# Optimization experiments

Measured on AMD Instinct MI355X. Metric: run time of the kernel, lower is better.

Reference implementation:

```python
import jax, jax.numpy as jnp
import numpy as np

N_EMBD = 1024
NUM_HEADS = 16
HEAD_SIZE = 64


def setup_inputs() -> dict:
    key = jax.random.key(0)
    ks = jax.random.split(key, 6)
    B, T, C, hs = 2, 2048, N_EMBD, HEAD_SIZE
    s = 0.02
    return {
        "x": jax.random.normal(ks[0], (B, T, C), dtype=jnp.float32),
        "Wk": jax.random.normal(ks[1], (hs, C), dtype=jnp.float32) * s,  # torch Linear weight [out,in]
        "Wv": jax.random.normal(ks[2], (hs, C), dtype=jnp.float32) * s,
        "Wq": jax.random.normal(ks[3], (C, C), dtype=jnp.float32) * s,
        "Wp": jax.random.normal(ks[4], (C, C), dtype=jnp.float32) * s,
        "bp": jax.random.normal(ks[5], (C,), dtype=jnp.float32) * s,
    }


def reference(x, Wk, Wv, Wq, Wp, bp):
    B, T, C = x.shape
    H, hs = NUM_HEADS, HEAD_SIZE
    k = x @ Wk.T                      # [B,T,hs]
    v = x @ Wv.T                      # [B,T,hs]
    q = x @ Wq.T                      # [B,T,C]
    # Faithful to torch: raw view of [B,T,C] -> [B,H,T,hs] (row-major reshape, not transpose)
    q = q.reshape(B, H, T, hs)
    k = k.reshape(B, 1, T, hs)
    v = v.reshape(B, 1, T, hs)
    att = jnp.einsum("bhqd,bhkd->bhqk", q, jnp.broadcast_to(k, (B, 1, T, hs))) * (hs ** -0.5)
    mask = jnp.tril(jnp.ones((T, T), dtype=bool))[None, None]  # [1,1,T,T]
    att = jnp.where(mask, att, -jnp.inf)
    att = jax.nn.softmax(att, axis=-1)
    y = jnp.einsum("bhqk,bhkd->bhqd", att, jnp.broadcast_to(v, (B, 1, T, hs)))  # [B,H,T,hs]
    y = jnp.transpose(y, (0, 2, 1, 3)).reshape(B, T, C)
    return y @ Wp.T + bp
```

## Files before the change

### kernel.cpp

```cpp
#include <hip/hip_runtime.h>
#include <cstddef>
#include <cstdint>

#define B_N 2
#define T_N 2048
#define C_N 1024
#define H_N 16
#define HS_N 64
#define M_N (B_N * T_N)

typedef __attribute__((ext_vector_type(8))) short bf16x8;
typedef __attribute__((ext_vector_type(4))) float f32x4;

#define QSCALE 0.18033688011112042f

__device__ __forceinline__ ushort f2bf(float f) {
    union { float f; uint32_t u; } v; v.f = f;
    uint32_t r = v.u + 0x7fffu + ((v.u >> 16) & 1u);
    return (ushort)(r >> 16);
}
__device__ __forceinline__ ushort f2bf_trunc(float f) {
    union { float f; uint32_t u; } v; v.f = f;
    return (ushort)(v.u >> 16);
}

#define GLL16(g, l)                                                         \
    __builtin_amdgcn_global_load_lds(                                       \
        (const __attribute__((address_space(1))) unsigned int*)(g),         \
        (__attribute__((address_space(3))) unsigned int*)(l), 16, 0, 0)

__global__ void cvt_all_kernel(const float* __restrict__ x,
                               const float* __restrict__ Wq,
                               const float* __restrict__ Wp,
                               const float* __restrict__ Wk,
                               const float* __restrict__ Wv,
                               ushort* __restrict__ xb,
                               ushort* __restrict__ Wqb,
                               ushort* __restrict__ Wpb,
                               ushort* __restrict__ Wkvb) {
    const int S0 = M_N * C_N / 4;
    const int S1 = S0 + C_N * C_N / 4;
    const int S2 = S1 + C_N * C_N / 4;
    const int S3 = S2 + HS_N * C_N / 4;
    const int S4 = S3 + HS_N * C_N / 4;
    const int stride = gridDim.x * blockDim.x;
    for (int i = blockIdx.x * blockDim.x + threadIdx.x; i < S4; i += stride) {
        const float* src; ushort* dst; int j; float sc = 1.f;
        if (i < S0)      { src = x;  dst = xb;   j = i; }
        else if (i < S1) { src = Wq; dst = Wqb;  j = i - S0; sc = QSCALE; }
        else if (i < S2) { src = Wp; dst = Wpb;  j = i - S1; }
        else if (i < S3) { src = Wk; dst = Wkvb; j = i - S2; }
        else             { src = Wv; dst = Wkvb + HS_N * C_N; j = i - S3; }
        const float4 f = ((const float4*)src)[j];
        ushort4 o;
        o.x = f2bf(f.x * sc); o.y = f2bf(f.y * sc);
        o.z = f2bf(f.z * sc); o.w = f2bf(f.w * sc);
        ((ushort4*)dst)[j] = o;
    }
}

template <int MODE>
__global__ __launch_bounds__(256, 2) void gemm_bf16(
    const ushort* __restrict__ A,
    const ushort* __restrict__ W,
    const float* __restrict__ bias,
    void* __restrict__ Cout,
    ushort* __restrict__ kb,
    ushort* __restrict__ vbt,
    int K)
{
    __shared__ ushort As[64 * 64];
    __shared__ ushort Bs[128 * 64];
    const int flat = blockIdx.x + (blockIdx.y << 6);
    const int m0 = (((flat & 7) << 3) | ((flat >> 3) & 7)) * 64;
    const int n0 = (flat >> 6) * 128;
    const int tid = threadIdx.x;
    const int wid = tid >> 6;
    const int lane = tid & 63;
    const int ln = lane & 15;
    const int quad = lane >> 4;
    const int wm = wid >> 1, wn = wid & 1;

    f32x4 acc[2][4];
    #pragma unroll
    for (int i = 0; i < 2; ++i)
        #pragma unroll
        for (int j = 0; j < 4; ++j)
            acc[i][j] = (f32x4){0.f, 0.f, 0.f, 0.f};

    const int srow = lane >> 3;
    const int schk = (lane & 7) ^ srow;

    for (int k0 = 0; k0 < K; k0 += 64) {
        __syncthreads();
        #pragma unroll
        for (int t = 0; t < 2; ++t) {
            const int seg = wid * 2 + t;
            GLL16(A + (size_t)(m0 + seg * 8 + srow) * K + k0 + schk * 8,
                  As + seg * 512);
        }
        #pragma unroll
        for (int t = 0; t < 4; ++t) {
            const int seg = wid * 4 + t;
            GLL16(W + (size_t)(n0 + seg * 8 + srow) * K + k0 + schk * 8,
                  Bs + seg * 512);
        }
        __syncthreads();

        #pragma unroll
        for (int hh = 0; hh < 2; ++hh) {
            bf16x8 af[2], bf[4];
            const int sw = ln & 7;
            #pragma unroll
            for (int i = 0; i < 2; ++i) {
                const int row = wm * 32 + i * 16 + ln;
                af[i] = *(const bf16x8*)&As[row * 64 + (((hh * 4 + quad) ^ sw) * 8)];
            }
            #pragma unroll
            for (int j = 0; j < 4; ++j) {
                const int row = wn * 64 + j * 16 + ln;
                bf[j] = *(const bf16x8*)&Bs[row * 64 + (((hh * 4 + quad) ^ sw) * 8)];
            }
            #pragma unroll
            for (int i = 0; i < 2; ++i)
                #pragma unroll
                for (int j = 0; j < 4; ++j)
                    acc[i][j] = __builtin_amdgcn_mfma_f32_16x16x32_bf16(
                        af[i], bf[j], acc[i][j], 0, 0, 0);
        }
    }

    if (MODE == 1 && n0 >= C_N) {
        #pragma unroll
        for (int i = 0; i < 2; ++i) {
            const int row0 = m0 + wm * 32 + i * 16 + quad * 4;
            #pragma unroll
            for (int j = 0; j < 4; ++j) {
                const int c2 = wn * 64 + j * 16 + ln;
                if (c2 >= 64) {
                    const int d = c2 - 64;
                    const int b = row0 >> 11;
                    const int t0 = row0 & 2047;
                    ushort4 pk;
                    pk.x = f2bf(acc[i][j][0]); pk.y = f2bf(acc[i][j][1]);
                    pk.z = f2bf(acc[i][j][2]); pk.w = f2bf(acc[i][j][3]);
                    *(ushort4*)&vbt[((size_t)b * 64 + d) * T_N + t0] = pk;
                } else {
                    #pragma unroll
                    for (int reg = 0; reg < 4; ++reg)
                        kb[(size_t)(row0 + reg) * 64 + c2] = f2bf(acc[i][j][reg]);
                }
            }
        }
        return;
    }

    #pragma unroll
    for (int i = 0; i < 2; ++i) {
        #pragma unroll
        for (int j = 0; j < 4; ++j) {
            const int col = n0 + wn * 64 + j * 16 + ln;
            const float bv = (MODE == 0) ? bias[col] : 0.f;
            #pragma unroll
            for (int reg = 0; reg < 4; ++reg) {
                const int row = m0 + wm * 32 + i * 16 + quad * 4 + reg;
                const float v = acc[i][j][reg] + bv;
                if (MODE == 0)
                    ((float*)Cout)[(size_t)row * C_N + col] = v;
                else
                    ((ushort*)Cout)[(size_t)row * C_N + col] = f2bf(v);
            }
        }
    }
}

__global__ __launch_bounds__(256, 2) void attn_mfma_kernel(
    const ushort* __restrict__ qb,
    const ushort* __restrict__ kb,
    const ushort* __restrict__ vbt,
    ushort* __restrict__ yb)
{
    __shared__ ushort Ks[64][72];
    __shared__ ushort Vt[64][72];
    __shared__ ushort Ps[4][16][72];

    const int bh = blockIdx.x;
    const int b = bh >> 4, h = bh & 15;
    const int p = blockIdx.y;
    const int qA0 = p * 64;
    const int qB0 = (31 - p) * 64;
    const int tid = threadIdx.x;
    const int wid = tid >> 6;
    const int lane = tid & 63;
    const int ln = lane & 15;
    const int quad = lane >> 4;

    const ushort* qstrip = qb + (size_t)b * T_N * C_N + (size_t)h * T_N * HS_N;
    const size_t rB = (size_t)(qB0 + wid * 16 + ln) * HS_N;
    const size_t rA = (size_t)(qA0 + wid * 16 + ln) * HS_N;
    bf16x8 qfB[2], qfA[2];
    qfB[0] = *(const bf16x8*)(qstrip + rB + quad * 8);
    qfB[1] = *(const bf16x8*)(qstrip + rB + 32 + quad * 8);
    qfA[0] = *(const bf16x8*)(qstrip + rA + quad * 8);
    qfA[1] = *(const bf16x8*)(qstrip + rA + 32 + quad * 8);

    f32x4 oB[4], oA[4];
    float lB = 0.f, lA = 0.f;
    #pragma unroll
    for (int nt = 0; nt < 4; ++nt) {
        oB[nt] = (f32x4){0.f, 0.f, 0.f, 0.f};
        oA[nt] = (f32x4){0.f, 0.f, 0.f, 0.f};
    }

    const ushort* kbase = kb + (size_t)b * T_N * HS_N;
    const ushort* vtbase = vbt + (size_t)b * HS_N * T_N;
    const int rs = tid >> 3;
    const int cs = tid & 7;

    int4 kc0, kc1, vc0, vc1;
    {
        kc0 = *(const int4*)(kbase + (size_t)rs * HS_N + cs * 8);
        kc1 = *(const int4*)(kbase + (size_t)(rs + 32) * HS_N + cs * 8);
        vc0 = *(const int4*)(vtbase + (size_t)rs * T_N + cs * 8);
        vc1 = *(const int4*)(vtbase + (size_t)(rs + 32) * T_N + cs * 8);
    }

    bf16x8 kf[4][2], vf[4][2];

    auto tile_compute = [&](const bf16x8* qf, f32x4* o, float& l,
                            int qt0, int k0) {
        const int qs0 = qt0 + wid * 16;
        const int qg = qs0 + ln;
        f32x4 sc[4];
        #pragma unroll
        for (int nt = 0; nt < 4; ++nt) {
            sc[nt] = (f32x4){0.f, 0.f, 0.f, 0.f};
            sc[nt] = __builtin_amdgcn_mfma_f32_16x16x32_bf16(
                kf[nt][0], qf[0], sc[nt], 0, 0, 0);
            sc[nt] = __builtin_amdgcn_mfma_f32_16x16x32_bf16(
                kf[nt][1], qf[1], sc[nt], 0, 0, 0);
        }
        const bool dg = (k0 + 63 > qs0);
        #pragma unroll
        for (int nt = 0; nt < 4; ++nt) {
            ushort pk[4];
            #pragma unroll
            for (int reg = 0; reg < 4; ++reg) {
                const int key = k0 + nt * 16 + quad * 4 + reg;
                float sv = sc[nt][reg];
                if (dg && key > qg) sv = -1e30f;
                const float pe = __builtin_amdgcn_exp2f(sv);
                l += pe;
                pk[reg] = f2bf_trunc(pe);
            }
            *(uint2*)&Ps[wid][ln][nt * 16 + quad * 4] = *(const uint2*)pk;
        }
        #pragma unroll
        for (int ks2 = 0; ks2 < 2; ++ks2) {
            const bf16x8 pf = *(const bf16x8*)&Ps[wid][ln][ks2 * 32 + quad * 8];
            #pragma unroll
            for (int nt = 0; nt < 4; ++nt)
                o[nt] = __builtin_amdgcn_mfma_f32_16x16x32_bf16(
                    pf, vf[nt][ks2], o[nt], 0, 0, 0);
        }
    };

    const int nkt = 32 - p;
    for (int kt = 0; kt < nkt; ++kt) {
        const int k0 = kt * 64;
        __syncthreads();
        *(int4*)&Ks[rs][cs * 8] = kc0;
        *(int4*)&Ks[rs + 32][cs * 8] = kc1;
        *(int4*)&Vt[rs][cs * 8] = vc0;
        *(int4*)&Vt[rs + 32][cs * 8] = vc1;
        __syncthreads();
        if (kt + 1 < nkt) {
            const int kn = k0 + 64;
            kc0 = *(const int4*)(kbase + (size_t)(kn + rs) * HS_N + cs * 8);
            kc1 = *(const int4*)(kbase + (size_t)(kn + rs + 32) * HS_N + cs * 8);
            vc0 = *(const int4*)(vtbase + (size_t)rs * T_N + kn + cs * 8);
            vc1 = *(const int4*)(vtbase + (size_t)(rs + 32) * T_N + kn + cs * 8);
        }
        #pragma unroll
        for (int nt = 0; nt < 4; ++nt) {
            kf[nt][0] = *(const bf16x8*)&Ks[nt * 16 + ln][quad * 8];
            kf[nt][1] = *(const bf16x8*)&Ks[nt * 16 + ln][32 + quad * 8];
            vf[nt][0] = *(const bf16x8*)&Vt[nt * 16 + ln][quad * 8];
            vf[nt][1] = *(const bf16x8*)&Vt[nt * 16 + ln][32 + quad * 8];
        }
        tile_compute(qfB, oB, lB, qB0, k0);
        if (kt <= p)
            tile_compute(qfA, oA, lA, qA0, k0);
    }

    #pragma unroll
    for (int t = 0; t < 2; ++t) {
        float l = t ? lA : lB;
        const f32x4* o = t ? oA : oB;
        const int qt0 = t ? qA0 : qB0;
        l += __shfl_xor(l, 16);
        l += __shfl_xor(l, 32);
        #pragma unroll
        for (int reg = 0; reg < 4; ++reg) {
            const float inv = 1.0f / __shfl(l, quad * 4 + reg);
            const int qg = qt0 + wid * 16 + quad * 4 + reg;
            ushort* yrow = yb + (size_t)b * T_N * C_N + (size_t)qg * C_N
                           + h * HS_N;
            #pragma unroll
            for (int nt = 0; nt < 4; ++nt)
                yrow[nt * 16 + ln] = f2bf(o[nt][reg] * inv);
        }
    }
}

extern "C" void kernel_launch(void* const* d_in, const int* in_sizes, int n_in,
                              void* d_out, int out_size, void* d_ws, size_t ws_size,
                              hipStream_t stream) {
    const float* x  = (const float*)d_in[0];
    const float* Wk = (const float*)d_in[1];
    const float* Wv = (const float*)d_in[2];
    const float* Wq = (const float*)d_in[3];
    const float* Wp = (const float*)d_in[4];
    const float* bp = (const float*)d_in[5];
    float* out = (float*)d_out;

    ushort* xb   = (ushort*)d_ws;
    ushort* qb   = xb   + (size_t)M_N * C_N;
    ushort* yb   = qb   + (size_t)M_N * C_N;
    ushort* kbw  = yb   + (size_t)M_N * C_N;
    ushort* vbt  = kbw  + (size_t)M_N * HS_N;
    ushort* Wqb  = vbt  + (size_t)B_N * HS_N * T_N;
    ushort* Wkvb = Wqb  + (size_t)C_N * C_N;
    ushort* Wpb  = Wkvb + (size_t)128 * C_N;

    cvt_all_kernel<<<1024, 256, 0, stream>>>(x, Wq, Wp, Wk, Wv,
                                             xb, Wqb, Wpb, Wkvb);

    gemm_bf16<1><<<dim3(M_N / 64, (C_N + 128) / 128), 256, 0, stream>>>(
        xb, Wqb, nullptr, qb, kbw, vbt, C_N);

    attn_mfma_kernel<<<dim3(B_N * H_N, 16), 256, 0, stream>>>(qb, kbw, vbt, yb);

    gemm_bf16<0><<<dim3(M_N / 64, C_N / 128), 256, 0, stream>>>(
        yb, Wpb, bp, out, nullptr, nullptr, C_N);
}
```

Measured before the change: 152.2 us.

## Restructure attention kernel: split-K across waves, async LDS staging, permlane P exchange

Rewrites the attention kernel so each block owns one 64-query tile and its four waves split each 128-key tile between them. The per-wave partial outputs and row sums are then reduced through LDS at the end. K/V tiles are double-buffered with global_load_lds using XOR-swizzled layouts. The P matrix is moved into MFMA operand layout via permlane swaps instead of an LDS round trip. This aims to cut LDS staging/sync overhead and improve load balance via a 32-block-per-head grid with ordered tile assignment, at the cost of a final cross-wave reduction and more registers for accumulators.

```diff
diff --git a/kernel.cpp b/kernel.cpp
--- a/kernel.cpp
+++ b/kernel.cpp
@@ -11,6 +11,8 @@
 
 typedef __attribute__((ext_vector_type(8))) short bf16x8;
 typedef __attribute__((ext_vector_type(4))) float f32x4;
+typedef __attribute__((ext_vector_type(4))) unsigned int u32x4;
+typedef __attribute__((ext_vector_type(2))) unsigned int u32x2;
 
 #define QSCALE 0.18033688011112042f
 
@@ -19,9 +21,9 @@
     uint32_t r = v.u + 0x7fffu + ((v.u >> 16) & 1u);
     return (ushort)(r >> 16);
 }
-__device__ __forceinline__ ushort f2bf_trunc(float f) {
-    union { float f; uint32_t u; } v; v.f = f;
-    return (ushort)(v.u >> 16);
+__device__ __forceinline__ unsigned pack2_trunc(float a, float b) {
+    union { float f; uint32_t u; } x, y; x.f = a; y.f = b;
+    return (x.u >> 16) | (y.u & 0xFFFF0000u);
 }
 
 #define GLL16(g, l)                                                         \
@@ -69,8 +71,8 @@
     ushort* __restrict__ vbt,
     int K)
 {
-    __shared__ ushort As[64 * 64];
-    __shared__ ushort Bs[128 * 64];
+    __shared__ __align__(16) ushort As[64 * 64];
+    __shared__ __align__(16) ushort Bs[128 * 64];
     const int flat = blockIdx.x + (blockIdx.y << 6);
     const int m0 = (((flat & 7) << 3) | ((flat >> 3) & 7)) * 64;
     const int n0 = (flat >> 6) * 128;
@@ -180,136 +182,189 @@
     const ushort* __restrict__ vbt,
     ushort* __restrict__ yb)
 {
-    __shared__ ushort Ks[64][72];
-    __shared__ ushort Vt[64][72];
-    __shared__ ushort Ps[4][16][72];
+    __shared__ __align__(16) ushort smem[32768];
 
     const int bh = blockIdx.x;
     const int b = bh >> 4, h = bh & 15;
-    const int p = blockIdx.y;
-    const int qA0 = p * 64;
-    const int qB0 = (31 - p) * 64;
+    const int yy = blockIdx.y;
+    const int qt = (yy < 8) ? 31 - yy : (yy < 16) ? yy - 8
+                 : (yy < 24) ? 39 - yy : yy - 16;
+    const int nkt = (qt >> 1) + 1;
+    const int qmax = qt * 64 + 63;
+
     const int tid = threadIdx.x;
-    const int wid = tid >> 6;
+    const int w = tid >> 6;
     const int lane = tid & 63;
     const int ln = lane & 15;
     const int quad = lane >> 4;
 
-    const ushort* qstrip = qb + (size_t)b * T_N * C_N + (size_t)h * T_N * HS_N;
-    const size_t rB = (size_t)(qB0 + wid * 16 + ln) * HS_N;
-    const size_t rA = (size_t)(qA0 + wid * 16 + ln) * HS_N;
-    bf16x8 qfB[2], qfA[2];
-    qfB[0] = *(const bf16x8*)(qstrip + rB + quad * 8);
-    qfB[1] = *(const bf16x8*)(qstrip + rB + 32 + quad * 8);
-    qfA[0] = *(const bf16x8*)(qstrip + rA + quad * 8);
-    qfA[1] = *(const bf16x8*)(qstrip + rA + 32 + quad * 8);
-
-    f32x4 oB[4], oA[4];
-    float lB = 0.f, lA = 0.f;
-    #pragma unroll
-    for (int nt = 0; nt < 4; ++nt) {
-        oB[nt] = (f32x4){0.f, 0.f, 0.f, 0.f};
-        oA[nt] = (f32x4){0.f, 0.f, 0.f, 0.f};
-    }
-
     const ushort* kbase = kb + (size_t)b * T_N * HS_N;
     const ushort* vtbase = vbt + (size_t)b * HS_N * T_N;
-    const int rs = tid >> 3;
-    const int cs = tid & 7;
-
-    int4 kc0, kc1, vc0, vc1;
+
+    bf16x8 qf[4][2];
     {
-        kc0 = *(const int4*)(kbase + (size_t)rs * HS_N + cs * 8);
-        kc1 = *(const int4*)(kbase + (size_t)(rs + 32) * HS_N + cs * 8);
-        vc0 = *(const int4*)(vtbase + (size_t)rs * T_N + cs * 8);
-        vc1 = *(const int4*)(vtbase + (size_t)(rs + 32) * T_N + cs * 8);
-    }
-
-    bf16x8 kf[4][2], vf[4][2];
-
-    auto tile_compute = [&](const bf16x8* qf, f32x4* o, float& l,
-                            int qt0, int k0) {
-        const int qs0 = qt0 + wid * 16;
-        const int qg = qs0 + ln;
-        f32x4 sc[4];
-        #pragma unroll
-        for (int nt = 0; nt < 4; ++nt) {
-            sc[nt] = (f32x4){0.f, 0.f, 0.f, 0.f};
-            sc[nt] = __builtin_amdgcn_mfma_f32_16x16x32_bf16(
-                kf[nt][0], qf[0], sc[nt], 0, 0, 0);
-            sc[nt] = __builtin_amdgcn_mfma_f32_16x16x32_bf16(
-                kf[nt][1], qf[1], sc[nt], 0, 0, 0);
-        }
-        const bool dg = (k0 + 63 > qs0);
-        #pragma unroll
-        for (int nt = 0; nt < 4; ++nt) {
-            ushort pk[4];
-            #pragma unroll
-            for (int reg = 0; reg < 4; ++reg) {
-                const int key = k0 + nt * 16 + quad * 4 + reg;
-                float sv = sc[nt][reg];
-                if (dg && key > qg) sv = -1e30f;
-                const float pe = __builtin_amdgcn_exp2f(sv);
-                l += pe;
-                pk[reg] = f2bf_trunc(pe);
-            }
-            *(uint2*)&Ps[wid][ln][nt * 16 + quad * 4] = *(const uint2*)pk;
-        }
-        #pragma unroll
-        for (int ks2 = 0; ks2 < 2; ++ks2) {
-            const bf16x8 pf = *(const bf16x8*)&Ps[wid][ln][ks2 * 32 + quad * 8];
-            #pragma unroll
-            for (int nt = 0; nt < 4; ++nt)
-                o[nt] = __builtin_amdgcn_mfma_f32_16x16x32_bf16(
-                    pf, vf[nt][ks2], o[nt], 0, 0, 0);
+        const ushort* qs_ = qb + (size_t)b * T_N * C_N
+                          + (size_t)h * T_N * HS_N
+                          + (size_t)(qt * 64) * HS_N;
+        #pragma unroll
+        for (int q4 = 0; q4 < 4; ++q4)
+            #pragma unroll
+            for (int kc = 0; kc < 2; ++kc)
+                qf[q4][kc] = *(const bf16x8*)(qs_ + (q4 * 16 + ln) * HS_N
+                                              + kc * 32 + quad * 8);
+    }
+
+    auto stage = [&](int buf, int k0) {
+        ushort* Ksb = smem + buf * 16384;
+        ushort* Vtb = Ksb + 8192;
+        #pragma unroll
+        for (int i = 0; i < 4; ++i) {
+            const int x = (i * 4 + w) * 64 + lane;
+            const int key = x >> 3, slk = x & 7;
+            GLL16(kbase + (size_t)(k0 + key) * HS_N + ((slk ^ (key & 7)) * 8),
+                  Ksb + (i * 4 + w) * 512);
+            const int d = x >> 4, slv = x & 15;
+            GLL16(vtbase + (size_t)d * T_N + k0 + ((slv ^ (d & 15)) * 8),
+                  Vtb + (i * 4 + w) * 512);
         }
     };
 
-    const int nkt = 32 - p;
+    f32x4 o[4][4];
+    #pragma unroll
+    for (int i = 0; i < 4; ++i)
+        #pragma unroll
+        for (int j = 0; j < 4; ++j)
+            o[i][j] = (f32x4){0.f, 0.f, 0.f, 0.f};
+    float lac[4] = {0.f, 0.f, 0.f, 0.f};
+
+    stage(0, 0);
+
     for (int kt = 0; kt < nkt; ++kt) {
-        const int k0 = kt * 64;
         __syncthreads();
-        *(int4*)&Ks[rs][cs * 8] = kc0;
-        *(int4*)&Ks[rs + 32][cs * 8] = kc1;
-        *(int4*)&Vt[rs][cs * 8] = vc0;
-        *(int4*)&Vt[rs + 32][cs * 8] = vc1;
+        if (kt + 1 < nkt) stage((kt + 1) & 1, (kt + 1) * 128);
+
+        const int k0 = kt * 128;
+        const bool dg = (kt == nkt - 1);
+        const int kw0 = k0 + w * 32;
+        if (dg && kw0 > qmax) continue;
+
+        const ushort* Ksb = smem + (kt & 1) * 16384;
+        const ushort* Vtb = Ksb + 8192;
+
+        bf16x8 kf[2][2], vf[4];
+        #pragma unroll
+        for (int nt = 0; nt < 2; ++nt)
+            #pragma unroll
+            for (int kc = 0; kc < 2; ++kc) {
+                const int key = w * 32 + nt * 16 + ln;
+                kf[nt][kc] = *(const bf16x8*)
+                    &Ksb[key * 64 + (((kc * 4 + quad) ^ (key & 7)) * 8)];
+            }
+        #pragma unroll
+        for (int db = 0; db < 4; ++db) {
+            const int d = db * 16 + ln;
+            vf[db] = *(const bf16x8*)
+                &Vtb[d * 128 + (((w * 4 + quad) ^ (d & 15)) * 8)];
+        }
+
+        f32x4 sc[2][4];
+        #pragma unroll
+        for (int nt = 0; nt < 2; ++nt)
+            #pragma unroll
+            for (int q4 = 0; q4 < 4; ++q4) {
+                f32x4 s = (f32x4){0.f, 0.f, 0.f, 0.f};
+                s = __builtin_amdgcn_mfma_f32_16x16x32_bf16(kf[nt][0], qf[q4][0], s, 0, 0, 0);
+                s = __builtin_amdgcn_mfma_f32_16x16x32_bf16(kf[nt][1], qf[q4][1], s, 0, 0, 0);
+                sc[nt][q4] = s;
+            }
+
+        unsigned pk[2][4][2];
+        #pragma unroll
+        for (int nt = 0; nt < 2; ++nt)
+            #pragma unroll
+            for (int q4 = 0; q4 < 4; ++q4) {
+                f32x4 s = sc[nt][q4];
+                if (dg) {
+                    const int qg = qt * 64 + q4 * 16 + ln;
+                    #pragma unroll
+                    for (int reg = 0; reg < 4; ++reg) {
+                        const int key = kw0 + nt * 16 + quad * 4 + reg;
+                        if (key > qg) s[reg] = -1e30f;
+                    }
+                }
+                const float p0 = __builtin_amdgcn_exp2f(s[0]);
+                const float p1 = __builtin_amdgcn_exp2f(s[1]);
+                const float p2 = __builtin_amdgcn_exp2f(s[2]);
+                const float p3 = __builtin_amdgcn_exp2f(s[3]);
+                lac[q4] += (p0 + p1) + (p2 + p3);
+                pk[nt][q4][0] = pack2_trunc(p0, p1);
+                pk[nt][q4][1] = pack2_trunc(p2, p3);
+            }
+
+        #pragma unroll
+        for (int q4 = 0; q4 < 4; ++q4) {
+            u32x2 ab0 = __builtin_amdgcn_permlane32_swap(pk[0][q4][0], pk[1][q4][0], false, false);
+            u32x2 rs0 = __builtin_amdgcn_permlane16_swap(ab0[0], ab0[1], false, false);
+            u32x2 ab1 = __builtin_amdgcn_permlane32_swap(pk[0][q4][1], pk[1][q4][1], false, false);
+            u32x2 rs1 = __builtin_amdgcn_permlane16_swap(ab1[0], ab1[1], false, false);
+            u32x4 pw;
+            pw[0] = rs0[0]; pw[1] = rs1[0]; pw[2] = rs0[1]; pw[3] = rs1[1];
+            const bf16x8 pf = __builtin_bit_cast(bf16x8, pw);
+            #pragma unroll
+            for (int db = 0; db < 4; ++db)
+                o[db][q4] = __builtin_amdgcn_mfma_f32_16x16x32_bf16(
+                    vf[db], pf, o[db][q4], 0, 0, 0);
+        }
+    }
+
+    #pragma unroll
+    for (int q4 = 0; q4 < 4; ++q4) {
+        lac[q4] += __shfl_xor(lac[q4], 16);
+        lac[q4] += __shfl_xor(lac[q4], 32);
+    }
+
+    float* Ored = (float*)smem;
+    const int qloc = 16 * w + (lane >> 2);
+    float inv = 0.f;
+
+    #pragma unroll
+    for (int pass = 0; pass < 2; ++pass) {
         __syncthreads();
-        if (kt + 1 < nkt) {
-            const int kn = k0 + 64;
-            kc0 = *(const int4*)(kbase + (size_t)(kn + rs) * HS_N + cs * 8);
-            kc1 = *(const int4*)(kbase + (size_t)(kn + rs + 32) * HS_N + cs * 8);
-            vc0 = *(const int4*)(vtbase + (size_t)rs * T_N + kn + cs * 8);
-            vc1 = *(const int4*)(vtbase + (size_t)(rs + 32) * T_N + kn + cs * 8);
-        }
-        #pragma unroll
-        for (int nt = 0; nt < 4; ++nt) {
-            kf[nt][0] = *(const bf16x8*)&Ks[nt * 16 + ln][quad * 8];
-            kf[nt][1] = *(const bf16x8*)&Ks[nt * 16 + ln][32 + quad * 8];
-            vf[nt][0] = *(const bf16x8*)&Vt[nt * 16 + ln][quad * 8];
-            vf[nt][1] = *(const bf16x8*)&Vt[nt * 16 + ln][32 + quad * 8];
-        }
-        tile_compute(qfB, oB, lB, qB0, k0);
-        if (kt <= p)
-            tile_compute(qfA, oA, lA, qA0, k0);
-    }
-
-    #pragma unroll
-    for (int t = 0; t < 2; ++t) {
-        float l = t ? lA : lB;
-        const f32x4* o = t ? oA : oB;
-        const int qt0 = t ? qA0 : qB0;
-        l += __shfl_xor(l, 16);
-        l += __shfl_xor(l, 32);
-        #pragma unroll
-        for (int reg = 0; reg < 4; ++reg) {
-            const float inv = 1.0f / __shfl(l, quad * 4 + reg);
-            const int qg = qt0 + wid * 16 + quad * 4 + reg;
-            ushort* yrow = yb + (size_t)b * T_N * C_N + (size_t)qg * C_N
-                           + h * HS_N;
-            #pragma unroll
-            for (int nt = 0; nt < 4; ++nt)
-                yrow[nt * 16 + ln] = f2bf(o[nt][reg] * inv);
-        }
+        #pragma unroll
+        for (int db2 = 0; db2 < 2; ++db2)
+            #pragma unroll
+            for (int q4 = 0; q4 < 4; ++q4)
+                *(f32x4*)&Ored[(w * 64 + q4 * 16 + ln) * 36 + db2 * 16 + quad * 4]
+                    = o[pass * 2 + db2][q4];
+        if (pass == 0 && quad == 0) {
+            #pragma unroll
+            for (int q4 = 0; q4 < 4; ++q4)
+                Ored[(w * 64 + q4 * 16 + ln) * 36 + 32] = lac[q4];
+        }
+        __syncthreads();
+
+        f32x4 a0 = (f32x4){0.f, 0.f, 0.f, 0.f};
+        f32x4 a1 = (f32x4){0.f, 0.f, 0.f, 0.f};
+        float ls = 0.f;
+        #pragma unroll
+        for (int v = 0; v < 4; ++v) {
+            const int base = (v * 64 + qloc) * 36;
+            a0 += *(const f32x4*)&Ored[base + (lane & 3) * 4];
+            a1 += *(const f32x4*)&Ored[base + 16 + (lane & 3) * 4];
+            if (pass == 0) ls += Ored[base + 32];
+        }
+        if (pass == 0) inv = 1.0f / ls;
+
+        const int qg = qt * 64 + qloc;
+        ushort* yrow = yb + ((size_t)b * T_N + qg) * C_N + h * HS_N
+                       + pass * 32 + (lane & 3) * 4;
+        ushort4 s0, s1;
+        s0.x = f2bf(a0[0] * inv); s0.y = f2bf(a0[1] * inv);
+        s0.z = f2bf(a0[2] * inv); s0.w = f2bf(a0[3] * inv);
+        s1.x = f2bf(a1[0] * inv); s1.y = f2bf(a1[1] * inv);
+        s1.z = f2bf(a1[2] * inv); s1.w = f2bf(a1[3] * inv);
+        *(ushort4*)yrow = s0;
+        *(ushort4*)(yrow + 16) = s1;
     }
 }
 
@@ -339,7 +394,7 @@
     gemm_bf16<1><<<dim3(M_N / 64, (C_N + 128) / 128), 256, 0, stream>>>(
         xb, Wqb, nullptr, qb, kbw, vbt, C_N);
 
-    attn_mfma_kernel<<<dim3(B_N * H_N, 16), 256, 0, stream>>>(qb, kbw, vbt, yb);
+    attn_mfma_kernel<<<dim3(B_N * H_N, 32), 256, 0, stream>>>(qb, kbw, vbt, yb);
 
     gemm_bf16<0><<<dim3(M_N / 64, C_N / 128), 256, 0, stream>>>(
         yb, Wpb, bp, out, nullptr, nullptr, C_N);
```

Measured after the change: 145.2 us. 4.6% less time.
